# Performance work log

Hardware: AMD Instinct MI355X
Metric: run time of the kernel (lower is better)

## Reference

```python
import jax, jax.numpy as jnp
import numpy as np
from jax import lax

N_NODES = 500
GAT_H = 32
HIDDEN = 128
B, S, E = 16, 64, 8000


def setup_inputs() -> dict:
    key = jax.random.key(0)
    ks = jax.random.split(key, 12)
    inp = {
        "x": jax.random.normal(ks[0], (B, S, N_NODES), dtype=jnp.float32),
        "edge_index": jax.random.randint(ks[1], (2, E), 0, N_NODES, dtype=jnp.int64),
        # GATConv params (in=1, out=GAT_H, heads=1, concat=False)
        "gat_w": jax.random.normal(ks[2], (GAT_H, 1), dtype=jnp.float32) * 0.5,
        "a_src": jax.random.normal(ks[3], (GAT_H,), dtype=jnp.float32) * 0.3,
        "a_dst": jax.random.normal(ks[4], (GAT_H,), dtype=jnp.float32) * 0.3,
        "gat_b": jax.random.normal(ks[5], (GAT_H,), dtype=jnp.float32) * 0.1,
        # LSTM params (input = GAT_H*N, hidden = HIDDEN), torch gate order i,f,g,o
        "w_ih": jax.random.normal(ks[6], (4 * HIDDEN, GAT_H * N_NODES), dtype=jnp.float32) * 0.01,
        "w_hh": jax.random.normal(ks[7], (4 * HIDDEN, HIDDEN), dtype=jnp.float32) * 0.05,
        "b_ih": jax.random.normal(ks[8], (4 * HIDDEN,), dtype=jnp.float32) * 0.05,
        "b_hh": jax.random.normal(ks[9], (4 * HIDDEN,), dtype=jnp.float32) * 0.05,
        # return head
        "head_w": jax.random.normal(ks[10], (N_NODES, HIDDEN), dtype=jnp.float32) * 0.05,
        "head_b": jax.random.normal(ks[11], (N_NODES,), dtype=jnp.float32) * 0.05,
    }
    return inp


def _gat_all(x, src, dst, gat_w, a_src, a_dst, gat_b):
    # x: [B,S,N]. Batched GAT over all B*S graphs sharing one edge structure.
    b, s, n = x.shape
    f = gat_w.shape[0]
    h = x[..., None] * gat_w[:, 0]                       # [B,S,N,F] (lin: W @ x, in=1)
    hf = h.reshape(b * s, n, f).transpose(1, 0, 2)       # [N,BS,F]
    al_s = hf @ a_src                                    # [N,BS]
    al_d = hf @ a_dst                                    # [N,BS]
    logits = jax.nn.leaky_relu(al_s[src] + al_d[dst], negative_slope=0.2)  # [Et,BS]
    m = jax.ops.segment_max(logits, dst, num_segments=n)                   # [N,BS]
    ex = jnp.exp(logits - m[dst])
    den = jax.ops.segment_sum(ex, dst, num_segments=n)
    alpha = ex / den[dst]                                # softmax over incoming edges
    msg = alpha[:, :, None] * hf[src]                    # [Et,BS,F]
    out = jax.ops.segment_sum(msg, dst, num_segments=n) + gat_b  # [N,BS,F]
    out = jax.nn.relu(out)
    return out.transpose(1, 0, 2).reshape(b, s, n * f)   # [B,S,N*F]


def reference(x, edge_index, gat_w, a_src, a_dst, gat_b, w_ih, w_hh, b_ih, b_hh, head_w, head_b):
    x = x.astype(jnp.float32)
    b, s, n = x.shape
    ei = edge_index.astype(jnp.int32)
    loop = jnp.arange(n, dtype=jnp.int32)               # GATConv adds self loops
    src = jnp.concatenate([ei[0], loop])
    dst = jnp.concatenate([ei[1], loop])

    lstm_in = _gat_all(x, src, dst, gat_w, a_src, a_dst, gat_b)  # [B,S,N*F]

    hdim = w_hh.shape[1]

    def step(carry, xt):
        h, c = carry
        gates = xt @ w_ih.T + h @ w_hh.T + b_ih + b_hh
        i, f, g, o = jnp.split(gates, 4, axis=-1)
        c = jax.nn.sigmoid(f) * c + jax.nn.sigmoid(i) * jnp.tanh(g)
        h = jax.nn.sigmoid(o) * jnp.tanh(c)
        return (h, c), None

    init = (jnp.zeros((b, hdim), jnp.float32), jnp.zeros((b, hdim), jnp.float32))
    (h_last, _), _ = lax.scan(step, init, lstm_in.transpose(1, 0, 2))  # scan over S

    return h_last @ head_w.T + head_b                    # [B,N]
```

## Files before the change

kernel.cpp:

```cpp
#include <hip/hip_runtime.h>
#include <hip/hip_bf16.h>
#include <hip/hip_fp16.h>

constexpr int NB = 16;
constexpr int SS = 64;
constexpr int BS = 1024;
constexpr int NN = 500;
constexpr int FF = 32;
constexpr int EE = 8000;
constexpr int ET = 8500;
constexpr int KK = 16000;
constexpr int HH = 128;
constexpr int GG = 512;
constexpr int KS = 16;

typedef __attribute__((ext_vector_type(8))) _Float16 f16x8;
typedef __attribute__((ext_vector_type(2))) _Float16 f16x2;
typedef __attribute__((ext_vector_type(4))) float f32x4;

__device__ __forceinline__ void gload_lds16(const void* g, void* l) {
    __builtin_amdgcn_global_load_lds((const __attribute__((address_space(1))) void*)g,
                                     (__attribute__((address_space(3))) void*)l, 16, 0, 0);
}

__device__ __forceinline__ float fast_sigmoid(float x) {
    return __builtin_amdgcn_rcpf(1.f + __expf(-x));
}

__device__ __forceinline__ float fdot2(f16x2 a, f16x2 b, float c) {
#if __has_builtin(__builtin_amdgcn_fdot2)
    return __builtin_amdgcn_fdot2(a, b, c, false);
#else
    return c + (float)a[0] * (float)b[0] + (float)a[1] * (float)b[1];
#endif
}

__device__ __forceinline__ void lds_barrier() {
    __builtin_amdgcn_sched_barrier(0);
    asm volatile("s_waitcnt lgkmcnt(0)");
    __builtin_amdgcn_sched_barrier(0);
    __builtin_amdgcn_s_barrier();
    __builtin_amdgcn_sched_barrier(0);
}

__global__ __launch_bounds__(256) void k_prep(const float* __restrict__ x, float* __restrict__ xt,
                                              const float* __restrict__ whh,
                                              _Float16* __restrict__ whh_h,
                                              const float* __restrict__ w_ih,
                                              _Float16* __restrict__ w_h) {
    __shared__ float tile[32][33];
    int bid = blockIdx.x;
    int tid = threadIdx.x;
    if (bid < 512) {
        int n0 = (bid & 15) * 32, bs0 = (bid >> 4) * 32;
        int tx = tid & 31, ty = tid >> 5;
#pragma unroll
        for (int i = 0; i < 4; ++i) {
            int n = n0 + tx, bs = bs0 + ty + i * 8;
            tile[ty + i * 8][tx] = (n < NN) ? x[bs * NN + n] : 0.f;
        }
        __syncthreads();
#pragma unroll
        for (int i = 0; i < 4; ++i) {
            int n = n0 + ty + i * 8, bs = bs0 + tx;
            if (n < NN) xt[n * BS + bs] = tile[tx][ty + i * 8];
        }
    } else if (bid < 768) {
        int idx = (bid - 512) * 256 + tid;
        whh_h[idx] = (_Float16)whh[idx];
    } else {
        int r = bid - 768;
        int g = r >> 3;
        int id = (r & 7) * 256 + tid;
        if (id < 2000) {
            int blk = id >> 3, sl = id & 7;
            int srcc = sl ^ (g & 7);
            const float* src = w_ih + (size_t)g * KK + blk * 64 + srcc * 8;
            float4 v0 = *(const float4*)src;
            float4 v1 = *(const float4*)(src + 4);
            union { __half2 h2[4]; uint4 q; } u;
            u.h2[0] = __floats2half2_rn(v0.x, v0.y);
            u.h2[1] = __floats2half2_rn(v0.z, v0.w);
            u.h2[2] = __floats2half2_rn(v1.x, v1.y);
            u.h2[3] = __floats2half2_rn(v1.z, v1.w);
            *(uint4*)(w_h + (size_t)g * KK + blk * 64 + sl * 8) = u.q;
        }
    }
}

__global__ __launch_bounds__(512) void k_graph(const int* __restrict__ ei,
                                               const float* __restrict__ gat_w,
                                               const float* __restrict__ a_src,
                                               const float* __restrict__ a_dst,
                                               int* __restrict__ offsets,
                                               int* __restrict__ esrc,
                                               float* __restrict__ scal) {
    __shared__ int cnt[512];
    __shared__ int sc[2][512];
    __shared__ int cur[512];
    int t = threadIdx.x;
    cnt[t] = 0;
    __syncthreads();
    for (int e = t; e < ET; e += 512) {
        int d = (e < EE) ? ei[EE + e] : (e - EE);
        atomicAdd(&cnt[d], 1);
    }
    __syncthreads();
    sc[0][t] = cnt[t];
    __syncthreads();
    int pb = 0;
    for (int off = 1; off < 512; off <<= 1) {
        int v = sc[pb][t];
        if (t >= off) v += sc[pb][t - off];
        sc[pb ^ 1][t] = v;
        pb ^= 1;
        __syncthreads();
    }
    int excl = sc[pb][t] - cnt[t];
    if (t <= NN) offsets[t] = excl;
    cur[t] = excl;
    if (t == 0) {
        float ws = 0.f, wd = 0.f;
        for (int f = 0; f < FF; ++f) {
            ws += gat_w[f] * a_src[f];
            wd += gat_w[f] * a_dst[f];
        }
        scal[0] = ws;
        scal[1] = wd;
    }
    __syncthreads();
    for (int e = t; e < ET; e += 512) {
        int sidx = (e < EE) ? ei[e] : (e - EE);
        int d = (e < EE) ? ei[EE + e] : (e - EE);
        int pos = atomicAdd(&cur[d], 1);
        esrc[pos] = sidx;
    }
}

__global__ void k_gat(const float* __restrict__ xt, const int* __restrict__ offsets,
                      const int* __restrict__ esrc, const float* __restrict__ scal,
                      float* __restrict__ s) {
    int n = blockIdx.y;
    int bs = blockIdx.x * 256 + threadIdx.x;
    float ws = scal[0], wd = scal[1];
    float xd = xt[n * BS + bs];
    float wdxd = wd * xd;
    int e0 = offsets[n], e1 = offsets[n + 1];
    float m = -1e30f, den = 0.f, num = 0.f;
    for (int j = e0; j < e1; ++j) {
        int sidx = esrc[j];
        float xs = xt[sidx * BS + bs];
        float z = ws * xs + wdxd;
        float l = (z > 0.f) ? z : 0.2f * z;
        if (l > m) {
            float r = __expf(m - l);
            den *= r;
            num *= r;
            m = l;
        }
        float p = __expf(l - m);
        den += p;
        num += p * xs;
    }
    s[n * BS + bs] = num / den;
}

__global__ __launch_bounds__(256, 2) void k_gemm_mfma(
    const _Float16* __restrict__ w_h, const float* __restrict__ s,
    const float* __restrict__ gat_w, const float* __restrict__ gat_b,
    float* __restrict__ G2) {
    __shared__ __align__(16) _Float16 Bs[2][128 * 64];
    __shared__ float s_lds[2][2][128];

    int tid = threadIdx.x;
    int lane = tid & 63;
    int w = tid >> 6;
    int wm = w >> 1, wn = w & 1;
    int bm = blockIdx.x, bn = blockIdx.y, ks = blockIdx.z;
    int bs0 = bm * 128, g0 = bn * 128;
    int step0 = (ks * 250) >> 4;
    int nst = (((ks + 1) * 250) >> 4) - step0;

    int fbase = (lane >> 4) * 8;
    float w8[8], b8[8];
#pragma unroll
    for (int j = 0; j < 8; ++j) {
        w8[j] = gat_w[fbase + j];
        b8[j] = gat_b[fbase + j];
    }

    f32x4 acc[4][4] = {};

    auto stageB = [&](int buf, int stepg) {
#pragma unroll
        for (int qq = 0; qq < 4; ++qq) {
            int q = w * 4 + qq;
            int row_local = q * 8 + (lane >> 3);
            int sl = lane & 7;
            const _Float16* srcp = w_h + (size_t)(g0 + row_local) * KK + stepg * 64 + sl * 8;
            gload_lds16(srcp, &Bs[buf][q * 512]);
        }
        int row = tid >> 7, col = tid & 127;
        int n = 2 * stepg + row;
        s_lds[buf][row][col] = s[n * BS + bs0 + col];
    };

    auto compute = [&](int buf) {
#pragma unroll
        for (int kh = 0; kh < 2; ++kh) {
            f16x8 bfrag[4];
#pragma unroll
            for (int fn = 0; fn < 4; ++fn) {
                int grow = wn * 64 + fn * 16 + (lane & 15);
                int c = kh * 4 + (lane >> 4);
                int slot = c ^ (grow & 7);
                bfrag[fn] = *(const f16x8*)&Bs[buf][grow * 64 + slot * 8];
            }
#pragma unroll
            for (int fm = 0; fm < 4; ++fm) {
                float sval = s_lds[buf][kh][wm * 64 + fm * 16 + (lane & 15)];
                union { f16x8 v; __half2 h2[4]; } af;
#pragma unroll
                for (int j2 = 0; j2 < 4; ++j2) {
                    float t0 = fmaf(sval, w8[2 * j2], b8[2 * j2]);
                    float t1 = fmaf(sval, w8[2 * j2 + 1], b8[2 * j2 + 1]);
                    t0 = t0 > 0.f ? t0 : 0.f;
                    t1 = t1 > 0.f ? t1 : 0.f;
                    af.h2[j2] = __floats2half2_rn(t0, t1);
                }
#pragma unroll
                for (int fn = 0; fn < 4; ++fn) {
                    acc[fm][fn] =
                        __builtin_amdgcn_mfma_f32_16x16x32_f16(af.v, bfrag[fn], acc[fm][fn], 0, 0, 0);
                }
            }
        }
    };

    stageB(0, step0);
    __syncthreads();
    for (int t = 0; t < nst; ++t) {
        if (t + 1 < nst) stageB((t + 1) & 1, step0 + t + 1);
        compute(t & 1);
        __syncthreads();
    }

    float* Gks = G2 + (size_t)ks * BS * GG;
#pragma unroll
    for (int fm = 0; fm < 4; ++fm) {
#pragma unroll
        for (int fn = 0; fn < 4; ++fn) {
            int bs = bs0 + wm * 64 + fm * 16 + ((lane >> 4) << 2);
            int g = g0 + wn * 64 + fn * 16 + (lane & 15);
            float* base = Gks + (size_t)bs * GG + g;
#pragma unroll
            for (int r = 0; r < 4; ++r) base[r * GG] = acc[fm][fn][r];
        }
    }
}

__global__ __launch_bounds__(256) void k_reduce(const float* __restrict__ G2,
                                                const float* __restrict__ b_ih,
                                                const float* __restrict__ b_hh,
                                                float* __restrict__ Xg) {
    int idx = blockIdx.x * 256 + threadIdx.x;
    int e = idx * 4;
    int g = e & (GG - 1);
    float4 acc = *(const float4*)&b_ih[g];
    float4 bh = *(const float4*)&b_hh[g];
    acc.x += bh.x; acc.y += bh.y; acc.z += bh.z; acc.w += bh.w;
#pragma unroll
    for (int p = 0; p < KS; ++p) {
        float4 v = *(const float4*)&G2[(size_t)p * BS * GG + e];
        acc.x += v.x; acc.y += v.y; acc.z += v.z; acc.w += v.w;
    }
    *(float4*)&Xg[e] = acc;
}

__global__ __launch_bounds__(512, 1) void k_lstm_dot2(const float* __restrict__ Xg,
                                                      const _Float16* __restrict__ whh_h,
                                                      const float* __restrict__ head_w,
                                                      const float* __restrict__ head_b,
                                                      float* __restrict__ out) {
    __shared__ __align__(16) _Float16 h_lds[HH];
    __shared__ __align__(16) float part[3 * HH * 4];
    __shared__ __align__(16) float hf[HH];

    int tid = threadIdx.x;
    int b = blockIdx.x;
    int d = tid & 127;
    int kc = tid >> 7;
    int k0 = kc * 32;

    union U8 { f16x8 v; f16x2 h[4]; };

    U8 w8[4][4];
#pragma unroll
    for (int q = 0; q < 4; ++q)
#pragma unroll
        for (int j = 0; j < 4; ++j)
            w8[q][j].v = *(const f16x8*)&whh_h[(q * HH + d) * HH + k0 + j * 8];
#pragma unroll
    for (int q = 0; q < 4; ++q)
#pragma unroll
        for (int j = 0; j < 4; ++j)
            asm volatile("" : "+v"(w8[q][j].v));

    if (tid < HH) h_lds[tid] = (_Float16)0.f;
    float c = 0.f;
    float xg[4] = {0.f, 0.f, 0.f, 0.f};
    if (kc == 0) {
#pragma unroll
        for (int q = 0; q < 4; ++q) xg[q] = Xg[(size_t)(b * SS) * GG + q * HH + d];
    }
    __syncthreads();

    for (int t = 0; t < SS; ++t) {
        U8 hh[4];
#pragma unroll
        for (int j = 0; j < 4; ++j) hh[j].v = *(const f16x8*)&h_lds[k0 + j * 8];
        float acc[4] = {0.f, 0.f, 0.f, 0.f};
#pragma unroll
        for (int j = 0; j < 4; ++j)
#pragma unroll
            for (int p = 0; p < 4; ++p) {
#pragma unroll
                for (int q = 0; q < 4; ++q)
                    acc[q] = fdot2(hh[j].h[p], w8[q][j].h[p], acc[q]);
            }
        if (kc) {
            float4 pv = {acc[0], acc[1], acc[2], acc[3]};
            *(float4*)&part[((kc - 1) * HH + d) * 4] = pv;
        }
        lds_barrier();
        if (kc == 0) {
            float4 p1 = *(const float4*)&part[(0 * HH + d) * 4];
            float4 p2 = *(const float4*)&part[(1 * HH + d) * 4];
            float4 p3 = *(const float4*)&part[(2 * HH + d) * 4];
            float ig = acc[0] + p1.x + p2.x + p3.x + xg[0];
            float fg = acc[1] + p1.y + p2.y + p3.y + xg[1];
            float gg = acc[2] + p1.z + p2.z + p3.z + xg[2];
            float og = acc[3] + p1.w + p2.w + p3.w + xg[3];
            int tn = (t + 1) & 63;
#pragma unroll
            for (int q = 0; q < 4; ++q)
                xg[q] = Xg[(size_t)(b * SS + tn) * GG + q * HH + d];
            float sf = fast_sigmoid(fg);
            float u = __expf(-ig);
            float wv = __expf(-2.f * fabsf(gg));
            float st = copysignf((1.f - wv) * __builtin_amdgcn_rcpf((1.f + u) * (1.f + wv)), gg);
            c = sf * c + st;
            float u2 = __expf(-og);
            float w2 = __expf(-2.f * fabsf(c));
            float h = copysignf((1.f - w2) * __builtin_amdgcn_rcpf((1.f + u2) * (1.f + w2)), c);
            h_lds[d] = (_Float16)h;
            if (t == SS - 1) hf[d] = h;
        }
        lds_barrier();
    }

    __syncthreads();
    if (tid < NN) {
        float a0 = head_b[tid], a1 = 0.f, a2 = 0.f, a3 = 0.f;
        const float4* w4 = (const float4*)&head_w[tid * HH];
        const float4* h4 = (const float4*)hf;
#pragma unroll
        for (int j4 = 0; j4 < 32; ++j4) {
            float4 wv = w4[j4];
            float4 hv = h4[j4];
            a0 = fmaf(wv.x, hv.x, a0);
            a1 = fmaf(wv.y, hv.y, a1);
            a2 = fmaf(wv.z, hv.z, a2);
            a3 = fmaf(wv.w, hv.w, a3);
        }
        out[b * NN + tid] = (a0 + a1) + (a2 + a3);
    }
}

extern "C" void kernel_launch(void* const* d_in, const int* in_sizes, int n_in, void* d_out,
                              int out_size, void* d_ws, size_t ws_size, hipStream_t stream) {
    const float* x = (const float*)d_in[0];
    const int* ei = (const int*)d_in[1];
    const float* gat_w = (const float*)d_in[2];
    const float* a_src = (const float*)d_in[3];
    const float* a_dst = (const float*)d_in[4];
    const float* gat_b = (const float*)d_in[5];
    const float* w_ih = (const float*)d_in[6];
    const float* w_hh = (const float*)d_in[7];
    const float* b_ih = (const float*)d_in[8];
    const float* b_hh = (const float*)d_in[9];
    const float* head_w = (const float*)d_in[10];
    const float* head_b = (const float*)d_in[11];
    float* out = (float*)d_out;

    char* ws = (char*)d_ws;
    float* xt = (float*)(ws + 0);
    float* s = (float*)(ws + 2048000u);
    float* G2 = (float*)(ws + 4096000u);
    _Float16* whh_h = (_Float16*)(ws + 37650432u);
    _Float16* w_h = (_Float16*)(ws + 37912576u);
    char* base2 = ws + 54296576u;
    int* offsets = (int*)(base2);
    int* esrc = (int*)(base2 + 4096);
    float* scal = (float*)(base2 + 45056);
    float* Xg = (float*)(ws + 0);

    k_prep<<<4864, 256, 0, stream>>>(x, xt, w_hh, whh_h, w_ih, w_h);
    k_graph<<<1, 512, 0, stream>>>(ei, gat_w, a_src, a_dst, offsets, esrc, scal);
    k_gat<<<dim3(BS / 256, NN), 256, 0, stream>>>(xt, offsets, esrc, scal, s);
    k_gemm_mfma<<<dim3(8, 4, KS), 256, 0, stream>>>(w_h, s, gat_w, gat_b, G2);
    k_reduce<<<512, 256, 0, stream>>>(G2, b_ih, b_hh, Xg);
    k_lstm_dot2<<<NB, 512, 0, stream>>>(Xg, whh_h, head_w, head_b, out);
}
```

Measured before the change: 131.6 us.

## Reduce LSTM gate partials with DPP lane adds and double-buffer hidden state

The recurrent LSTM kernel now maps the four K-chunks of each hidden unit to adjacent lanes. Partial gate sums are combined with DPP quad-permute adds instead of an LDS partial buffer, which removes one LDS barrier per timestep. The hidden state is ping-ponged between two LDS buffers so a single barrier per step is enough. In exchange, all four lanes redundantly compute the gate nonlinearities, and every lane now loads the Xg values.

```diff
diff --git a/kernel.cpp b/kernel.cpp
--- a/kernel.cpp
+++ b/kernel.cpp
@@ -31,8 +31,16 @@
 #if __has_builtin(__builtin_amdgcn_fdot2)
     return __builtin_amdgcn_fdot2(a, b, c, false);
 #else
-    return c + (float)a[0] * (float)b[0] + (float)a[1] * (float)b[1];
+    float r;
+    asm("v_dot2_f32_f16 %0, %1, %2, %3" : "=v"(r) : "v"(a), "v"(b), "v"(c));
+    return r;
 #endif
+}
+
+template <int CTRL>
+__device__ __forceinline__ float dpp_add(float x) {
+    int y = __builtin_amdgcn_mov_dpp(__float_as_int(x), CTRL, 0xF, 0xF, true);
+    return x + __int_as_float(y);
 }
 
 __device__ __forceinline__ void lds_barrier() {
@@ -277,19 +285,19 @@
     *(float4*)&Xg[e] = acc;
 }
 
-__global__ __launch_bounds__(512, 1) void k_lstm_dot2(const float* __restrict__ Xg,
+__global__ __launch_bounds__(512, 1) void k_lstm_shfl(const float* __restrict__ Xg,
                                                       const _Float16* __restrict__ whh_h,
                                                       const float* __restrict__ head_w,
                                                       const float* __restrict__ head_b,
                                                       float* __restrict__ out) {
-    __shared__ __align__(16) _Float16 h_lds[HH];
-    __shared__ __align__(16) float part[3 * HH * 4];
+    __shared__ __align__(16) _Float16 hb0[HH];
+    __shared__ __align__(16) _Float16 hb1[HH];
     __shared__ __align__(16) float hf[HH];
 
     int tid = threadIdx.x;
     int b = blockIdx.x;
-    int d = tid & 127;
-    int kc = tid >> 7;
+    int d = tid >> 2;
+    int kc = tid & 3;
     int k0 = kc * 32;
 
     union U8 { f16x8 v; f16x2 h[4]; };
@@ -306,19 +314,17 @@
         for (int j = 0; j < 4; ++j)
             asm volatile("" : "+v"(w8[q][j].v));
 
-    if (tid < HH) h_lds[tid] = (_Float16)0.f;
+    if (tid < HH) hb0[tid] = (_Float16)0.f;
     float c = 0.f;
-    float xg[4] = {0.f, 0.f, 0.f, 0.f};
-    if (kc == 0) {
-#pragma unroll
-        for (int q = 0; q < 4; ++q) xg[q] = Xg[(size_t)(b * SS) * GG + q * HH + d];
-    }
-    __syncthreads();
-
-    for (int t = 0; t < SS; ++t) {
+    float xg[4];
+#pragma unroll
+    for (int q = 0; q < 4; ++q) xg[q] = Xg[(size_t)(b * SS) * GG + q * HH + d];
+    __syncthreads();
+
+    auto lstm_step = [&](const _Float16* hr, _Float16* hw, int t) {
         U8 hh[4];
 #pragma unroll
-        for (int j = 0; j < 4; ++j) hh[j].v = *(const f16x8*)&h_lds[k0 + j * 8];
+        for (int j = 0; j < 4; ++j) hh[j].v = *(const f16x8*)&hr[k0 + j * 8];
         float acc[4] = {0.f, 0.f, 0.f, 0.f};
 #pragma unroll
         for (int j = 0; j < 4; ++j)
@@ -328,35 +334,37 @@
                 for (int q = 0; q < 4; ++q)
                     acc[q] = fdot2(hh[j].h[p], w8[q][j].h[p], acc[q]);
             }
-        if (kc) {
-            float4 pv = {acc[0], acc[1], acc[2], acc[3]};
-            *(float4*)&part[((kc - 1) * HH + d) * 4] = pv;
+#pragma unroll
+        for (int q = 0; q < 4; ++q) {
+            acc[q] = dpp_add<0xB1>(acc[q]);
+            acc[q] = dpp_add<0x4E>(acc[q]);
+        }
+        float ig = acc[0] + xg[0];
+        float fg = acc[1] + xg[1];
+        float gg = acc[2] + xg[2];
+        float og = acc[3] + xg[3];
+        int tn = (t + 1) & 63;
+#pragma unroll
+        for (int q = 0; q < 4; ++q)
+            xg[q] = Xg[(size_t)(b * SS + tn) * GG + q * HH + d];
+        float sf = fast_sigmoid(fg);
+        float u = __expf(-ig);
+        float wv = __expf(-2.f * fabsf(gg));
+        float st = copysignf((1.f - wv) * __builtin_amdgcn_rcpf((1.f + u) * (1.f + wv)), gg);
+        c = sf * c + st;
+        float u2 = __expf(-og);
+        float w2 = __expf(-2.f * fabsf(c));
+        float h = copysignf((1.f - w2) * __builtin_amdgcn_rcpf((1.f + u2) * (1.f + w2)), c);
+        if (kc == 0) {
+            hw[d] = (_Float16)h;
+            if (t == SS - 1) hf[d] = h;
         }
         lds_barrier();
-        if (kc == 0) {
-            float4 p1 = *(const float4*)&part[(0 * HH + d) * 4];
-            float4 p2 = *(const float4*)&part[(1 * HH + d) * 4];
-            float4 p3 = *(const float4*)&part[(2 * HH + d) * 4];
-            float ig = acc[0] + p1.x + p2.x + p3.x + xg[0];
-            float fg = acc[1] + p1.y + p2.y + p3.y + xg[1];
-            float gg = acc[2] + p1.z + p2.z + p3.z + xg[2];
-            float og = acc[3] + p1.w + p2.w + p3.w + xg[3];
-            int tn = (t + 1) & 63;
-#pragma unroll
-            for (int q = 0; q < 4; ++q)
-                xg[q] = Xg[(size_t)(b * SS + tn) * GG + q * HH + d];
-            float sf = fast_sigmoid(fg);
-            float u = __expf(-ig);
-            float wv = __expf(-2.f * fabsf(gg));
-            float st = copysignf((1.f - wv) * __builtin_amdgcn_rcpf((1.f + u) * (1.f + wv)), gg);
-            c = sf * c + st;
-            float u2 = __expf(-og);
-            float w2 = __expf(-2.f * fabsf(c));
-            float h = copysignf((1.f - w2) * __builtin_amdgcn_rcpf((1.f + u2) * (1.f + w2)), c);
-            h_lds[d] = (_Float16)h;
-            if (t == SS - 1) hf[d] = h;
-        }
-        lds_barrier();
+    };
+
+    for (int tt = 0; tt < SS; tt += 2) {
+        lstm_step(hb0, hb1, tt);
+        lstm_step(hb1, hb0, tt + 1);
     }
 
     __syncthreads();
@@ -410,5 +418,5 @@
     k_gat<<<dim3(BS / 256, NN), 256, 0, stream>>>(xt, offsets, esrc, scal, s);
     k_gemm_mfma<<<dim3(8, 4, KS), 256, 0, stream>>>(w_h, s, gat_w, gat_b, G2);
     k_reduce<<<512, 256, 0, stream>>>(G2, b_ih, b_hh, Xg);
-    k_lstm_dot2<<<NB, 512, 0, stream>>>(Xg, whh_h, head_w, head_b, out);
-}
+    k_lstm_shfl<<<NB, 512, 0, stream>>>(Xg, whh_h, head_w, head_b, out);
+}
```

New measurement: 125.4 us. -4.7%, faster.
